# Kernel optimization log

Hardware: AMD Instinct MI355X
Metric: run time of the kernel (lower is better)

## Reference

```python
import jax, jax.numpy as jnp
import numpy as np

W_IMG = 512
H_IMG = 512
D_MODEL = 192
N_FREQ = 8
LN_EPS = 1e-5


def _fourier_pe(coords_norm):
    # coords_norm: [B,K,2] in [0,1); returns [B,K,4*N_FREQ]
    freqs = 2.0 ** jnp.arange(N_FREQ, dtype=jnp.float32)  # [F]
    two_pi = 2.0 * jnp.pi
    x = coords_norm[..., 0:1] * freqs * two_pi  # [B,K,F]
    y = coords_norm[..., 1:2] * freqs * two_pi
    return jnp.concatenate([jnp.sin(x), jnp.cos(x), jnp.sin(y), jnp.cos(y)], axis=-1)


def _bilinear_sample(feat, gx, gy):
    # feat: [B,C,H,W]; gx,gy: [B,K] normalized coords in [-1,1], align_corners=True
    B, C, H, W = feat.shape
    ix = (gx + 1.0) * 0.5 * (W - 1)
    iy = (gy + 1.0) * 0.5 * (H - 1)
    ix0 = jnp.floor(ix)
    iy0 = jnp.floor(iy)
    wx = ix - ix0  # [B,K]
    wy = iy - iy0
    x0 = jnp.clip(ix0.astype(jnp.int32), 0, W - 1)
    x1 = jnp.clip(ix0.astype(jnp.int32) + 1, 0, W - 1)
    y0 = jnp.clip(iy0.astype(jnp.int32), 0, H - 1)
    y1 = jnp.clip(iy0.astype(jnp.int32) + 1, 0, H - 1)
    b = jnp.arange(B)[:, None]  # [B,1] broadcast against [B,K]
    g = lambda y, x: feat[b, :, y, x]  # [B,K,C]
    out = (g(y0, x0) * ((1 - wx) * (1 - wy))[..., None]
           + g(y0, x1) * (wx * (1 - wy))[..., None]
           + g(y1, x0) * ((1 - wx) * wy)[..., None]
           + g(y1, x1) * (wx * wy)[..., None])
    return out  # [B,K,C]


def setup_inputs() -> dict:
    key = jax.random.key(0)
    ks = jax.random.split(key, 16)
    B, K = 8, 4096
    # pixel coordinates in [0, W_IMG-1] x [0, H_IMG-1]
    u = jax.random.uniform(ks[0], (B, K, 2), dtype=jnp.float32)
    coords = u * jnp.array([W_IMG - 1, H_IMG - 1], dtype=jnp.float32)
    L1 = jax.random.normal(ks[1], (B, D_MODEL, 128, 128), dtype=jnp.float32)
    L2 = jax.random.normal(ks[2], (B, D_MODEL, 64, 64), dtype=jnp.float32)
    L3 = jax.random.normal(ks[3], (B, D_MODEL, 32, 32), dtype=jnp.float32)
    L4 = jax.random.normal(ks[4], (B, D_MODEL, 16, 16), dtype=jnp.float32)
    d_in = D_MODEL * 4 + 4 * N_FREQ  # 800
    Wseed_w = jax.random.normal(ks[5], (D_MODEL, d_in), dtype=jnp.float32) / np.sqrt(d_in)
    Wseed_b = jnp.zeros((D_MODEL,), dtype=jnp.float32)
    ln_g = jnp.ones((D_MODEL,), dtype=jnp.float32)
    ln_b = jnp.zeros((D_MODEL,), dtype=jnp.float32)
    Wpos_w = jax.random.normal(ks[6], (D_MODEL, 4 * N_FREQ), dtype=jnp.float32) / np.sqrt(4 * N_FREQ)
    Wpos_b = jnp.zeros((D_MODEL,), dtype=jnp.float32)
    return {"coords": coords, "L1": L1, "L2": L2, "L3": L3, "L4": L4,
            "Wseed_w": Wseed_w, "Wseed_b": Wseed_b, "ln_g": ln_g, "ln_b": ln_b,
            "Wpos_w": Wpos_w, "Wpos_b": Wpos_b}


def reference(coords, L1, L2, L3, L4, Wseed_w, Wseed_b, ln_g, ln_b, Wpos_w, Wpos_b):
    B, K, _ = coords.shape
    # normalized grid in [-1,1] (x uses W, y uses H), align_corners=True convention
    gx = 2.0 * coords[..., 0] / (W_IMG - 1) - 1.0  # [B,K]
    gy = 2.0 * coords[..., 1] / (H_IMG - 1) - 1.0
    center_grid = jnp.stack([gx, gy], axis=-1).reshape(B, K, 1, 2)
    coords_norm = coords / jnp.array([W_IMG, H_IMG], dtype=jnp.float32)
    pe_q = _fourier_pe(coords_norm)  # [B,K,32]
    f1 = _bilinear_sample(L1, gx, gy)
    f2 = _bilinear_sample(L2, gx, gy)
    f3 = _bilinear_sample(L3, gx, gy)
    f4 = _bilinear_sample(L4, gx, gy)
    x = jnp.concatenate([f1, f2, f3, f4, pe_q], axis=-1)  # [B,K,800]
    seed = x @ Wseed_w.T + Wseed_b
    mu = jnp.mean(seed, axis=-1, keepdims=True)
    var = jnp.mean((seed - mu) ** 2, axis=-1, keepdims=True)
    seed = (seed - mu) / jnp.sqrt(var + LN_EPS) * ln_g + ln_b
    pos = pe_q @ Wpos_w.T + Wpos_b
    return (seed, pos, center_grid)
```

## Files before the change

kernel.cpp:

```cpp
#include <hip/hip_runtime.h>
#include <stdint.h>

typedef unsigned short u16;
typedef short s16x8 __attribute__((ext_vector_type(8)));
typedef float f32x4 __attribute__((ext_vector_type(4)));
typedef uint32_t u32x4 __attribute__((ext_vector_type(4)));

__device__ __forceinline__ u16 f2bf(float f) {
  union { float f; uint32_t u; } a; a.f = f;
  uint32_t u = a.u;
  uint32_t r = (u + 0x7fffu + ((u >> 16) & 1u)) >> 16;
  return (u16)r;
}
__device__ __forceinline__ float bf2f(uint32_t hbits) {
  union { uint32_t u; float f; } a; a.u = hbits << 16;
  return a.f;
}

__global__ __launch_bounds__(256) void prep_all(
    const float* __restrict__ L1, const float* __restrict__ L2,
    const float* __restrict__ L3, const float* __restrict__ L4,
    const float* __restrict__ ws_w, const float* __restrict__ wp_w,
    u16* __restrict__ T1, u16* __restrict__ T2,
    u16* __restrict__ T3, u16* __restrict__ T4,
    u16* __restrict__ dWs, u16* __restrict__ dWp) {
  const int bid = blockIdx.x;
  const int t = threadIdx.x;

  if (bid >= 2720) {
    int t0 = (bid - 2720) * 256 + t;
    for (int i = t0; i < 39936; i += 8192) {
      const float* s; u16* d; int off;
      if (i < 38400) { s = ws_w; d = dWs; off = 4 * i; }
      else           { s = wp_w; d = dWp; off = 4 * (i - 38400); }
      f32x4 v = *(const f32x4*)(s + off);
      uint2 o;
      o.x = (uint32_t)f2bf(v.x) | ((uint32_t)f2bf(v.y) << 16);
      o.y = (uint32_t)f2bf(v.z) | ((uint32_t)f2bf(v.w) << 16);
      *(uint2*)(d + off) = o;
    }
    return;
  }

  const float* src; u16* dst; int HW, tiles, rel;
  if (bid < 2048)      { src = L1; dst = T1; HW = 16384; tiles = 256; rel = bid; }
  else if (bid < 2560) { src = L2; dst = T2; HW = 4096;  tiles = 64;  rel = bid - 2048; }
  else if (bid < 2688) { src = L3; dst = T3; HW = 1024;  tiles = 16;  rel = bid - 2560; }
  else                 { src = L4; dst = T4; HW = 256;   tiles = 4;   rel = bid - 2688; }
  const int b = rel / tiles, hw0 = (rel % tiles) * 64;

  __shared__ uint32_t tileD[96 * 65];
  const float* sb = src + (size_t)b * 192 * HW + hw0;
  for (int i = 0; i < 6; ++i) {
    int idx = i * 256 + t;
    int c2 = idx >> 4, hw4 = idx & 15;
    f32x4 a = *(const f32x4*)(sb + (size_t)(2 * c2) * HW + hw4 * 4);
    f32x4 c = *(const f32x4*)(sb + (size_t)(2 * c2 + 1) * HW + hw4 * 4);
    uint32_t* w = &tileD[c2 * 65 + hw4 * 4];
    w[0] = (uint32_t)f2bf(a.x) | ((uint32_t)f2bf(c.x) << 16);
    w[1] = (uint32_t)f2bf(a.y) | ((uint32_t)f2bf(c.y) << 16);
    w[2] = (uint32_t)f2bf(a.z) | ((uint32_t)f2bf(c.z) << 16);
    w[3] = (uint32_t)f2bf(a.w) | ((uint32_t)f2bf(c.w) << 16);
  }
  __syncthreads();
  uint32_t* d = (uint32_t*)(dst + ((size_t)b * HW + hw0) * 192);
  for (int i = 0; i < 24; ++i) {
    int e = i * 256 + t;
    int hw = e / 96, c2 = e - hw * 96;
    d[hw * 96 + c2] = tileD[c2 * 65 + hw];
  }
}

__global__ __launch_bounds__(256, 5) void seed_main(
    const float* __restrict__ coords,
    const u16* __restrict__ T1, const u16* __restrict__ T2,
    const u16* __restrict__ T3, const u16* __restrict__ T4,
    const u16* __restrict__ Wseed, const u16* __restrict__ Wpos,
    const float* __restrict__ seed_b, const float* __restrict__ ln_g,
    const float* __restrict__ ln_b, const float* __restrict__ pos_b,
    float* __restrict__ out_seed, float* __restrict__ out_pos,
    float* __restrict__ out_cg) {

  __shared__ __align__(16) u16 xt[16 * 808];
  __shared__ float mu_s[16], rs_s[16];

  const int t = threadIdx.x;
  const int gp0 = blockIdx.x * 16;
  const int b = gp0 >> 12;

  if (t < 32) {
    int p = t >> 1, xy = t & 1;
    float c = coords[(gp0 + p) * 2 + xy];
    out_cg[(gp0 + p) * 2 + xy] = c * (2.0f / 511.0f) - 1.0f;
  }
  for (int i = 0; i < 2; ++i) {
    int e = i * 256 + t;
    int p = e >> 5, j = e & 31;
    float c = coords[(gp0 + p) * 2 + ((j >> 4) & 1)] * (1.0f / 512.0f);
    float v = c * (float)(1 << (j & 7));
    float a = (v - floorf(v)) * 6.283185307179586f;
    float r = (j & 8) ? __cosf(a) : __sinf(a);
    xt[p * 808 + 768 + j] = f2bf(r);
  }

  const u16* B1 = T1 + (size_t)b * 16384 * 192;
  const u16* B2 = T2 + (size_t)b * 4096 * 192;
  const u16* B3 = T3 + (size_t)b * 1024 * 192;
  const u16* B4 = T4 + (size_t)b * 256 * 192;
  for (int i = 0; i < 6; ++i) {
    int e = i * 256 + t;
    int c4 = e % 24;
    int plv = e / 24;
    int lv = plv & 3, p = plv >> 2;
    float cx = coords[(gp0 + p) * 2 + 0];
    float cy = coords[(gp0 + p) * 2 + 1];
    float gx = cx * (2.0f / 511.0f) - 1.0f;
    float gy = cy * (2.0f / 511.0f) - 1.0f;
    int Wl = 128 >> lv;
    float ix = (gx + 1.0f) * 0.5f * (float)(Wl - 1);
    float iy = (gy + 1.0f) * 0.5f * (float)(Wl - 1);
    float fx = floorf(ix), fy = floorf(iy);
    float wx = ix - fx, wy = iy - fy;
    int x0 = (int)fx, y0 = (int)fy;
    int x1 = min(max(x0 + 1, 0), Wl - 1), y1 = min(max(y0 + 1, 0), Wl - 1);
    x0 = min(max(x0, 0), Wl - 1); y0 = min(max(y0, 0), Wl - 1);
    const u16* base = (lv == 0) ? B1 : (lv == 1) ? B2 : (lv == 2) ? B3 : B4;
    int cc = c4 * 8;
    u32x4 q00 = *(const u32x4*)(base + (y0 * Wl + x0) * 192 + cc);
    u32x4 q01 = *(const u32x4*)(base + (y0 * Wl + x1) * 192 + cc);
    u32x4 q10 = *(const u32x4*)(base + (y1 * Wl + x0) * 192 + cc);
    u32x4 q11 = *(const u32x4*)(base + (y1 * Wl + x1) * 192 + cc);
    float w00 = (1.0f - wx) * (1.0f - wy), w01 = wx * (1.0f - wy);
    float w10 = (1.0f - wx) * wy,          w11 = wx * wy;
    u32x4 o;
#pragma unroll
    for (int k = 0; k < 4; ++k) {
      float lo = bf2f(q00[k] & 0xffff) * w00 + bf2f(q01[k] & 0xffff) * w01 +
                 bf2f(q10[k] & 0xffff) * w10 + bf2f(q11[k] & 0xffff) * w11;
      float hi = bf2f(q00[k] >> 16) * w00 + bf2f(q01[k] >> 16) * w01 +
                 bf2f(q10[k] >> 16) * w10 + bf2f(q11[k] >> 16) * w11;
      o[k] = (uint32_t)f2bf(lo) | ((uint32_t)f2bf(hi) << 16);
    }
    *(u32x4*)(xt + p * 808 + lv * 192 + cc) = o;
  }
  __syncthreads();

  const int lid = t & 63, wv = t >> 6;
  const int quad = lid >> 4, mrow = lid & 15;
  const int nt0 = wv * 3;

  f32x4 accS[3], accP[3];
#pragma unroll
  for (int j = 0; j < 3; ++j) { accS[j] = (f32x4)0.0f; accP[j] = (f32x4)0.0f; }

  s16x8 a_last;
#pragma unroll 1
  for (int kc = 0; kc < 25; ++kc) {
    int ko = kc * 32 + quad * 8;
    s16x8 a = *(const s16x8*)(xt + mrow * 808 + ko);
#pragma unroll
    for (int j = 0; j < 3; ++j) {
      int n = (nt0 + j) * 16 + mrow;
      s16x8 bw = *(const s16x8*)(Wseed + n * 800 + ko);
      accS[j] = __builtin_amdgcn_mfma_f32_16x16x32_bf16(a, bw, accS[j], 0, 0, 0);
    }
    if (kc == 24) a_last = a;
  }
#pragma unroll
  for (int j = 0; j < 3; ++j) {
    int n = (nt0 + j) * 16 + mrow;
    s16x8 bw = *(const s16x8*)(Wpos + n * 32 + quad * 8);
    accP[j] = __builtin_amdgcn_mfma_f32_16x16x32_bf16(a_last, bw, accP[j], 0, 0, 0);
  }

#pragma unroll
  for (int j = 0; j < 3; ++j) {
    int n = (nt0 + j) * 16 + mrow;
    float pb = pos_b[n];
#pragma unroll
    for (int r = 0; r < 4; ++r)
      out_pos[(size_t)(gp0 + quad * 4 + r) * 192 + n] = accP[j][r] + pb;
  }

  __syncthreads();
  float* preLN = (float*)xt;
#pragma unroll
  for (int j = 0; j < 3; ++j) {
    int n = (nt0 + j) * 16 + mrow;
    float sb = seed_b[n];
#pragma unroll
    for (int r = 0; r < 4; ++r)
      preLN[(quad * 4 + r) * 193 + n] = accS[j][r] + sb;
  }
  __syncthreads();

  {
    int r = t >> 4, g = t & 15;
    float s = 0.0f, sq = 0.0f;
#pragma unroll
    for (int i = 0; i < 12; ++i) {
      float v = preLN[r * 193 + g * 12 + i];
      s += v; sq += v * v;
    }
#pragma unroll
    for (int d = 8; d > 0; d >>= 1) {
      s += __shfl_down(s, d, 16);
      sq += __shfl_down(sq, d, 16);
    }
    if (g == 0) {
      float mu = s * (1.0f / 192.0f);
      float var = sq * (1.0f / 192.0f) - mu * mu;
      mu_s[r] = mu;
      rs_s[r] = 1.0f / sqrtf(var + 1e-5f);
    }
  }
  __syncthreads();

  for (int i = 0; i < 12; ++i) {
    int e = i * 256 + t;
    int r = e / 192, n = e - r * 192;
    float v = (preLN[r * 193 + n] - mu_s[r]) * rs_s[r] * ln_g[n] + ln_b[n];
    out_seed[(size_t)(gp0 + r) * 192 + n] = v;
  }
}

extern "C" void kernel_launch(void* const* d_in, const int* in_sizes, int n_in,
                              void* d_out, int out_size, void* d_ws, size_t ws_size,
                              hipStream_t stream) {
  const float* coords  = (const float*)d_in[0];
  const float* L1      = (const float*)d_in[1];
  const float* L2      = (const float*)d_in[2];
  const float* L3      = (const float*)d_in[3];
  const float* L4      = (const float*)d_in[4];
  const float* Wseed_w = (const float*)d_in[5];
  const float* Wseed_b = (const float*)d_in[6];
  const float* ln_g    = (const float*)d_in[7];
  const float* ln_b    = (const float*)d_in[8];
  const float* Wpos_w  = (const float*)d_in[9];
  const float* Wpos_b  = (const float*)d_in[10];

  u16* T1  = (u16*)d_ws;
  u16* T2  = T1 + (size_t)8 * 16384 * 192;
  u16* T3  = T2 + (size_t)8 * 4096 * 192;
  u16* T4  = T3 + (size_t)8 * 1024 * 192;
  u16* Wsd = T4 + (size_t)8 * 256 * 192;
  u16* Wps = Wsd + 153600;

  prep_all<<<2752, 256, 0, stream>>>(L1, L2, L3, L4, Wseed_w, Wpos_w,
                                     T1, T2, T3, T4, Wsd, Wps);

  float* out_seed = (float*)d_out;
  float* out_pos  = out_seed + (size_t)32768 * 192;
  float* out_cg   = out_pos  + (size_t)32768 * 192;

  seed_main<<<2048, 256, 0, stream>>>(coords, T1, T2, T3, T4, Wsd, Wps,
                                      Wseed_b, ln_g, ln_b, Wpos_b,
                                      out_seed, out_pos, out_cg);
}
```

Measured before the change: 278.0 us.

## Use packed bf16 conversion, wider stores, restructured gather, and unrolled MFMA loop

Replaces the manual bf16 rounding with the packed __float22bfloat162_rn intrinsic in prep and gather. The transpose write-out now stores two words per thread as uint2. The gather gives each thread one point and level and loops over six channel chunks, so coordinate and weight math is done once per thread instead of six times. The GEMM k-loop precomputes weight row pointers and unrolls by 5 to expose more loads. Occupancy hint drops from 5 to 4 waves per SIMD to leave more registers for the unrolled code.

```diff
diff --git a/kernel.cpp b/kernel.cpp
--- a/kernel.cpp
+++ b/kernel.cpp
@@ -1,4 +1,5 @@
 #include <hip/hip_runtime.h>
+#include <hip/hip_bf16.h>
 #include <stdint.h>
 
 typedef unsigned short u16;
@@ -6,11 +7,16 @@
 typedef float f32x4 __attribute__((ext_vector_type(4)));
 typedef uint32_t u32x4 __attribute__((ext_vector_type(4)));
 
+__device__ __forceinline__ uint32_t pack_bf16(float lo, float hi) {
+  float2 f; f.x = lo; f.y = hi;
+  __hip_bfloat162 h = __float22bfloat162_rn(f);
+  union { __hip_bfloat162 h; uint32_t u; } c; c.h = h;
+  return c.u;
+}
 __device__ __forceinline__ u16 f2bf(float f) {
   union { float f; uint32_t u; } a; a.f = f;
   uint32_t u = a.u;
-  uint32_t r = (u + 0x7fffu + ((u >> 16) & 1u)) >> 16;
-  return (u16)r;
+  return (u16)((u + 0x7fffu + ((u >> 16) & 1u)) >> 16);
 }
 __device__ __forceinline__ float bf2f(uint32_t hbits) {
   union { uint32_t u; float f; } a; a.u = hbits << 16;
@@ -35,8 +41,8 @@
       else           { s = wp_w; d = dWp; off = 4 * (i - 38400); }
       f32x4 v = *(const f32x4*)(s + off);
       uint2 o;
-      o.x = (uint32_t)f2bf(v.x) | ((uint32_t)f2bf(v.y) << 16);
-      o.y = (uint32_t)f2bf(v.z) | ((uint32_t)f2bf(v.w) << 16);
+      o.x = pack_bf16(v.x, v.y);
+      o.y = pack_bf16(v.z, v.w);
       *(uint2*)(d + off) = o;
     }
     return;
@@ -57,21 +63,24 @@
     f32x4 a = *(const f32x4*)(sb + (size_t)(2 * c2) * HW + hw4 * 4);
     f32x4 c = *(const f32x4*)(sb + (size_t)(2 * c2 + 1) * HW + hw4 * 4);
     uint32_t* w = &tileD[c2 * 65 + hw4 * 4];
-    w[0] = (uint32_t)f2bf(a.x) | ((uint32_t)f2bf(c.x) << 16);
-    w[1] = (uint32_t)f2bf(a.y) | ((uint32_t)f2bf(c.y) << 16);
-    w[2] = (uint32_t)f2bf(a.z) | ((uint32_t)f2bf(c.z) << 16);
-    w[3] = (uint32_t)f2bf(a.w) | ((uint32_t)f2bf(c.w) << 16);
+    w[0] = pack_bf16(a.x, c.x);
+    w[1] = pack_bf16(a.y, c.y);
+    w[2] = pack_bf16(a.z, c.z);
+    w[3] = pack_bf16(a.w, c.w);
   }
   __syncthreads();
   uint32_t* d = (uint32_t*)(dst + ((size_t)b * HW + hw0) * 192);
-  for (int i = 0; i < 24; ++i) {
+  for (int i = 0; i < 12; ++i) {
     int e = i * 256 + t;
-    int hw = e / 96, c2 = e - hw * 96;
-    d[hw * 96 + c2] = tileD[c2 * 65 + hw];
-  }
-}
-
-__global__ __launch_bounds__(256, 5) void seed_main(
+    int hw = e / 48, cp = e - hw * 48;
+    uint2 v;
+    v.x = tileD[(cp * 2) * 65 + hw];
+    v.y = tileD[(cp * 2 + 1) * 65 + hw];
+    *(uint2*)(d + hw * 96 + cp * 2) = v;
+  }
+}
+
+__global__ __launch_bounds__(256, 4) void seed_main(
     const float* __restrict__ coords,
     const u16* __restrict__ T1, const u16* __restrict__ T2,
     const u16* __restrict__ T3, const u16* __restrict__ T4,
@@ -103,15 +112,14 @@
     xt[p * 808 + 768 + j] = f2bf(r);
   }
 
-  const u16* B1 = T1 + (size_t)b * 16384 * 192;
-  const u16* B2 = T2 + (size_t)b * 4096 * 192;
-  const u16* B3 = T3 + (size_t)b * 1024 * 192;
-  const u16* B4 = T4 + (size_t)b * 256 * 192;
-  for (int i = 0; i < 6; ++i) {
-    int e = i * 256 + t;
-    int c4 = e % 24;
-    int plv = e / 24;
+  {
+    const u16* B1 = T1 + (size_t)b * 16384 * 192;
+    const u16* B2 = T2 + (size_t)b * 4096 * 192;
+    const u16* B3 = T3 + (size_t)b * 1024 * 192;
+    const u16* B4 = T4 + (size_t)b * 256 * 192;
+    int plv = t >> 2;
     int lv = plv & 3, p = plv >> 2;
+    int c4b = t & 3;
     float cx = coords[(gp0 + p) * 2 + 0];
     float cy = coords[(gp0 + p) * 2 + 1];
     float gx = cx * (2.0f / 511.0f) - 1.0f;
@@ -125,23 +133,31 @@
     int x1 = min(max(x0 + 1, 0), Wl - 1), y1 = min(max(y0 + 1, 0), Wl - 1);
     x0 = min(max(x0, 0), Wl - 1); y0 = min(max(y0, 0), Wl - 1);
     const u16* base = (lv == 0) ? B1 : (lv == 1) ? B2 : (lv == 2) ? B3 : B4;
-    int cc = c4 * 8;
-    u32x4 q00 = *(const u32x4*)(base + (y0 * Wl + x0) * 192 + cc);
-    u32x4 q01 = *(const u32x4*)(base + (y0 * Wl + x1) * 192 + cc);
-    u32x4 q10 = *(const u32x4*)(base + (y1 * Wl + x0) * 192 + cc);
-    u32x4 q11 = *(const u32x4*)(base + (y1 * Wl + x1) * 192 + cc);
+    const u16* b00 = base + (y0 * Wl + x0) * 192;
+    const u16* b01 = base + (y0 * Wl + x1) * 192;
+    const u16* b10 = base + (y1 * Wl + x0) * 192;
+    const u16* b11 = base + (y1 * Wl + x1) * 192;
     float w00 = (1.0f - wx) * (1.0f - wy), w01 = wx * (1.0f - wy);
     float w10 = (1.0f - wx) * wy,          w11 = wx * wy;
-    u32x4 o;
-#pragma unroll
-    for (int k = 0; k < 4; ++k) {
-      float lo = bf2f(q00[k] & 0xffff) * w00 + bf2f(q01[k] & 0xffff) * w01 +
-                 bf2f(q10[k] & 0xffff) * w10 + bf2f(q11[k] & 0xffff) * w11;
-      float hi = bf2f(q00[k] >> 16) * w00 + bf2f(q01[k] >> 16) * w01 +
-                 bf2f(q10[k] >> 16) * w10 + bf2f(q11[k] >> 16) * w11;
-      o[k] = (uint32_t)f2bf(lo) | ((uint32_t)f2bf(hi) << 16);
-    }
-    *(u32x4*)(xt + p * 808 + lv * 192 + cc) = o;
+    u16* dstp = xt + p * 808 + lv * 192;
+#pragma unroll
+    for (int i = 0; i < 6; ++i) {
+      int cc = (c4b + 4 * i) * 8;
+      u32x4 q00 = *(const u32x4*)(b00 + cc);
+      u32x4 q01 = *(const u32x4*)(b01 + cc);
+      u32x4 q10 = *(const u32x4*)(b10 + cc);
+      u32x4 q11 = *(const u32x4*)(b11 + cc);
+      u32x4 o;
+#pragma unroll
+      for (int k = 0; k < 4; ++k) {
+        float lo = bf2f(q00[k] & 0xffff) * w00 + bf2f(q01[k] & 0xffff) * w01 +
+                   bf2f(q10[k] & 0xffff) * w10 + bf2f(q11[k] & 0xffff) * w11;
+        float hi = bf2f(q00[k] >> 16) * w00 + bf2f(q01[k] >> 16) * w01 +
+                   bf2f(q10[k] >> 16) * w10 + bf2f(q11[k] >> 16) * w11;
+        o[k] = pack_bf16(lo, hi);
+      }
+      *(u32x4*)(dstp + cc) = o;
+    }
   }
   __syncthreads();
 
@@ -153,17 +169,22 @@
 #pragma unroll
   for (int j = 0; j < 3; ++j) { accS[j] = (f32x4)0.0f; accP[j] = (f32x4)0.0f; }
 
+  const u16* wp0 = Wseed + (size_t)((nt0 + 0) * 16 + mrow) * 800 + quad * 8;
+  const u16* wp1 = wp0 + 16 * 800;
+  const u16* wp2 = wp1 + 16 * 800;
+  const u16* arow = xt + mrow * 808 + quad * 8;
+
   s16x8 a_last;
-#pragma unroll 1
+#pragma unroll 5
   for (int kc = 0; kc < 25; ++kc) {
-    int ko = kc * 32 + quad * 8;
-    s16x8 a = *(const s16x8*)(xt + mrow * 808 + ko);
-#pragma unroll
-    for (int j = 0; j < 3; ++j) {
-      int n = (nt0 + j) * 16 + mrow;
-      s16x8 bw = *(const s16x8*)(Wseed + n * 800 + ko);
-      accS[j] = __builtin_amdgcn_mfma_f32_16x16x32_bf16(a, bw, accS[j], 0, 0, 0);
-    }
+    int ko = kc * 32;
+    s16x8 a = *(const s16x8*)(arow + ko);
+    s16x8 b0 = *(const s16x8*)(wp0 + ko);
+    s16x8 b1 = *(const s16x8*)(wp1 + ko);
+    s16x8 b2 = *(const s16x8*)(wp2 + ko);
+    accS[0] = __builtin_amdgcn_mfma_f32_16x16x32_bf16(a, b0, accS[0], 0, 0, 0);
+    accS[1] = __builtin_amdgcn_mfma_f32_16x16x32_bf16(a, b1, accS[1], 0, 0, 0);
+    accS[2] = __builtin_amdgcn_mfma_f32_16x16x32_bf16(a, b2, accS[2], 0, 0, 0);
     if (kc == 24) a_last = a;
   }
 #pragma unroll
```

Measured after the change: 273.9 us. No clear change (-1.5%).
